# Kernel optimization log

Measured on AMD Instinct MI355X. Metric: run time of the kernel, lower is better.

Reference implementation:

```python
import jax, jax.numpy as jnp
import numpy as np

N, C, H, W = 1, 128, 512, 512
CH = C // 2  # channels seen by each 1x1 conv


def setup_inputs() -> dict:
    key = jax.random.key(0)
    ks = jax.random.split(key, 6)
    return {
        "lst": jax.random.normal(ks[0], (N, C, H, W), dtype=jnp.float32),
        "gui": jax.random.normal(ks[1], (N, C, H, W), dtype=jnp.float32),
        "w1": jax.random.normal(ks[2], (CH, CH), dtype=jnp.float32) * 0.05,  # conv1 weight (out,in) of 1x1 kernel
        "b1": jax.random.normal(ks[3], (CH,), dtype=jnp.float32) * 0.05,
        "w2": jax.random.normal(ks[4], (CH, CH), dtype=jnp.float32) * 0.05,  # conv2 weight
        "b2": jax.random.normal(ks[5], (CH,), dtype=jnp.float32) * 0.05,
        "p": 2,
    }


def _conv1x1(x, w, b):
    # x: [N, CH, H, W]; 1x1 conv == per-pixel channel mixing GEMM
    return jnp.einsum('oc,nchw->nohw', w, x) + b[None, :, None, None]


def reference(lst, gui, w1, b1, w2, b2, p):
    # channel_mask = arange(C) % p == 0 selects channels 0, p, 2p, ... -> strided slice [:, ::p]
    # Exchanged channels: out_lst gets conv2(gui_masked), out_gui gets conv1(lst_masked).
    # Unmasked channels pass through unchanged (out initialized as copy of input).
    out_lst = lst.at[:, ::p].set(_conv1x1(gui[:, ::p], w2, b2))
    out_gui = gui.at[:, ::p].set(_conv1x1(lst[:, ::p], w1, b1))
    return (out_lst, out_gui)
```

## Files before the change

### kernel.cpp

```cpp
#include <hip/hip_runtime.h>

#define HW (512 * 512)
#define CH 64
#define CONV_BLOCKS 1024
#define COPY_BLOCKS 4096
#define COPY_THREADS (COPY_BLOCKS * 256)
#define COPY_R 4

__global__ __launch_bounds__(256) void fused_exchange_kernel(
    const float* __restrict__ lst, const float* __restrict__ gui,
    const float* __restrict__ w1, const float* __restrict__ b1,
    const float* __restrict__ w2, const float* __restrict__ b2,
    float* __restrict__ out_lst, float* __restrict__ out_gui)
{
    const int b = blockIdx.x;

    if (b < CONV_BLOCKS) {
        const int pix = b * 256 + threadIdx.x;

        {
            float acc[CH];
            #pragma unroll
            for (int k = 0; k < CH; ++k) acc[k] = b2[k];

            for (int cc = 0; cc < CH; cc += 8) {
                float x[8];
                #pragma unroll
                for (int j = 0; j < 8; ++j)
                    x[j] = gui[(size_t)(2 * (cc + j)) * HW + pix];
                #pragma unroll
                for (int k = 0; k < CH; ++k) {
                    const float* wr = w2 + k * CH + cc;
                    float a = acc[k];
                    a = fmaf(wr[0], x[0], a);
                    a = fmaf(wr[1], x[1], a);
                    a = fmaf(wr[2], x[2], a);
                    a = fmaf(wr[3], x[3], a);
                    a = fmaf(wr[4], x[4], a);
                    a = fmaf(wr[5], x[5], a);
                    a = fmaf(wr[6], x[6], a);
                    a = fmaf(wr[7], x[7], a);
                    acc[k] = a;
                }
            }
            #pragma unroll
            for (int k = 0; k < CH; ++k)
                out_lst[(size_t)(2 * k) * HW + pix] = acc[k];
        }

        {
            float acc[CH];
            #pragma unroll
            for (int k = 0; k < CH; ++k) acc[k] = b1[k];

            for (int cc = 0; cc < CH; cc += 8) {
                float x[8];
                #pragma unroll
                for (int j = 0; j < 8; ++j)
                    x[j] = lst[(size_t)(2 * (cc + j)) * HW + pix];
                #pragma unroll
                for (int k = 0; k < CH; ++k) {
                    const float* wr = w1 + k * CH + cc;
                    float a = acc[k];
                    a = fmaf(wr[0], x[0], a);
                    a = fmaf(wr[1], x[1], a);
                    a = fmaf(wr[2], x[2], a);
                    a = fmaf(wr[3], x[3], a);
                    a = fmaf(wr[4], x[4], a);
                    a = fmaf(wr[5], x[5], a);
                    a = fmaf(wr[6], x[6], a);
                    a = fmaf(wr[7], x[7], a);
                    acc[k] = a;
                }
            }
            #pragma unroll
            for (int k = 0; k < CH; ++k)
                out_gui[(size_t)(2 * k) * HW + pix] = acc[k];
        }
    } else {
        const int t = (b - CONV_BLOCKS) * 256 + threadIdx.x;
        const float4* l4  = (const float4*)lst;
        const float4* g4  = (const float4*)gui;
        float4* ol4 = (float4*)out_lst;
        float4* og4 = (float4*)out_gui;

        #pragma unroll
        for (int r = 0; r < COPY_R; ++r) {
            const int idx = t + r * COPY_THREADS;
            const int c   = idx >> 16;
            const int j   = idx & 0xFFFF;
            const int off = ((2 * c + 1) << 16) + j;
            ol4[off] = l4[off];
            og4[off] = g4[off];
        }
    }
}

extern "C" void kernel_launch(void* const* d_in, const int* in_sizes, int n_in,
                              void* d_out, int out_size, void* d_ws, size_t ws_size,
                              hipStream_t stream) {
    const float* lst = (const float*)d_in[0];
    const float* gui = (const float*)d_in[1];
    const float* w1  = (const float*)d_in[2];
    const float* b1  = (const float*)d_in[3];
    const float* w2  = (const float*)d_in[4];
    const float* b2  = (const float*)d_in[5];

    float* out_lst = (float*)d_out;
    float* out_gui = out_lst + (size_t)128 * HW;

    fused_exchange_kernel<<<CONV_BLOCKS + COPY_BLOCKS, 256, 0, stream>>>(
        lst, gui, w1, b1, w2, b2, out_lst, out_gui);
}
```

Measured before the change: 553.2 us.

## Split conv output channels across waves with float2 pixels and uniform copy work

Restructures the fused kernel so each block handles 128 pixels, with each of four waves computing 16 output channels over two pixels per lane (float2). Weight addresses become wave-uniform via readfirstlane, so weights can live in scalar loads. Input channel loads are software-prefetched one chunk ahead. Every block now does both convs plus a slice of the passthrough copy instead of splitting conv and copy blocks, and launch bounds ask for higher occupancy. Each wave re-reads the same inputs, four times per block, which trades redundant loads for far lower register pressure.

```diff
diff --git a/kernel.cpp b/kernel.cpp
--- a/kernel.cpp
+++ b/kernel.cpp
@@ -2,96 +2,83 @@
 
 #define HW (512 * 512)
 #define CH 64
-#define CONV_BLOCKS 1024
-#define COPY_BLOCKS 4096
-#define COPY_THREADS (COPY_BLOCKS * 256)
-#define COPY_R 4
+#define NBLK 2048
+#define PIXB 128
+#define COPY_R 16
 
-__global__ __launch_bounds__(256) void fused_exchange_kernel(
+__global__ __launch_bounds__(256, 4) void fused_exchange_kernel(
     const float* __restrict__ lst, const float* __restrict__ gui,
     const float* __restrict__ w1, const float* __restrict__ b1,
     const float* __restrict__ w2, const float* __restrict__ b2,
     float* __restrict__ out_lst, float* __restrict__ out_gui)
 {
-    const int b = blockIdx.x;
+    const int b    = blockIdx.x;
+    const int tid  = threadIdx.x;
+    const int lane = tid & 63;
+    const int kg   = __builtin_amdgcn_readfirstlane(tid >> 6);
+    const int pix  = b * PIXB + lane * 2;
 
-    if (b < CONV_BLOCKS) {
-        const int pix = b * 256 + threadIdx.x;
+    auto conv_pass = [&](const float* __restrict__ src, const float* __restrict__ w,
+                         const float* __restrict__ bias, float* __restrict__ dst) {
+        const float* wbase = w + (size_t)(kg * 16) * CH;
 
-        {
-            float acc[CH];
-            #pragma unroll
-            for (int k = 0; k < CH; ++k) acc[k] = b2[k];
-
-            for (int cc = 0; cc < CH; cc += 8) {
-                float x[8];
-                #pragma unroll
-                for (int j = 0; j < 8; ++j)
-                    x[j] = gui[(size_t)(2 * (cc + j)) * HW + pix];
-                #pragma unroll
-                for (int k = 0; k < CH; ++k) {
-                    const float* wr = w2 + k * CH + cc;
-                    float a = acc[k];
-                    a = fmaf(wr[0], x[0], a);
-                    a = fmaf(wr[1], x[1], a);
-                    a = fmaf(wr[2], x[2], a);
-                    a = fmaf(wr[3], x[3], a);
-                    a = fmaf(wr[4], x[4], a);
-                    a = fmaf(wr[5], x[5], a);
-                    a = fmaf(wr[6], x[6], a);
-                    a = fmaf(wr[7], x[7], a);
-                    acc[k] = a;
-                }
-            }
-            #pragma unroll
-            for (int k = 0; k < CH; ++k)
-                out_lst[(size_t)(2 * k) * HW + pix] = acc[k];
+        float2 acc[16];
+        #pragma unroll
+        for (int k = 0; k < 16; ++k) {
+            const float bb = bias[kg * 16 + k];
+            acc[k].x = bb; acc[k].y = bb;
         }
 
-        {
-            float acc[CH];
+        float2 x[8];
+        #pragma unroll
+        for (int j = 0; j < 8; ++j)
+            x[j] = *(const float2*)(src + (size_t)(2 * j) * HW + pix);
+
+        auto fma_chunk = [&](int c0, const float2* xv) {
             #pragma unroll
-            for (int k = 0; k < CH; ++k) acc[k] = b1[k];
+            for (int k = 0; k < 16; ++k) {
+                const float* wr = wbase + k * CH + c0;
+                float ax = acc[k].x, ay = acc[k].y;
+                #pragma unroll
+                for (int j = 0; j < 8; ++j) {
+                    ax = fmaf(wr[j], xv[j].x, ax);
+                    ay = fmaf(wr[j], xv[j].y, ay);
+                }
+                acc[k].x = ax; acc[k].y = ay;
+            }
+        };
 
-            for (int cc = 0; cc < CH; cc += 8) {
-                float x[8];
-                #pragma unroll
-                for (int j = 0; j < 8; ++j)
-                    x[j] = lst[(size_t)(2 * (cc + j)) * HW + pix];
-                #pragma unroll
-                for (int k = 0; k < CH; ++k) {
-                    const float* wr = w1 + k * CH + cc;
-                    float a = acc[k];
-                    a = fmaf(wr[0], x[0], a);
-                    a = fmaf(wr[1], x[1], a);
-                    a = fmaf(wr[2], x[2], a);
-                    a = fmaf(wr[3], x[3], a);
-                    a = fmaf(wr[4], x[4], a);
-                    a = fmaf(wr[5], x[5], a);
-                    a = fmaf(wr[6], x[6], a);
-                    a = fmaf(wr[7], x[7], a);
-                    acc[k] = a;
-                }
-            }
+        for (int c0 = 0; c0 < CH - 8; c0 += 8) {
+            float2 xn[8];
             #pragma unroll
-            for (int k = 0; k < CH; ++k)
-                out_gui[(size_t)(2 * k) * HW + pix] = acc[k];
+            for (int j = 0; j < 8; ++j)
+                xn[j] = *(const float2*)(src + (size_t)(2 * (c0 + 8 + j)) * HW + pix);
+            fma_chunk(c0, x);
+            #pragma unroll
+            for (int j = 0; j < 8; ++j) x[j] = xn[j];
         }
-    } else {
-        const int t = (b - CONV_BLOCKS) * 256 + threadIdx.x;
-        const float4* l4  = (const float4*)lst;
-        const float4* g4  = (const float4*)gui;
-        float4* ol4 = (float4*)out_lst;
-        float4* og4 = (float4*)out_gui;
+        fma_chunk(CH - 8, x);
+
+        #pragma unroll
+        for (int k = 0; k < 16; ++k)
+            *(float2*)(dst + (size_t)(2 * (kg * 16 + k)) * HW + pix) = acc[k];
+    };
+
+    conv_pass(gui, w2, b2, out_lst);
+    conv_pass(lst, w1, b1, out_gui);
+
+    {
+        const float4* src = (b < 1024) ? (const float4*)lst : (const float4*)gui;
+        float4*       dst = (b < 1024) ? (float4*)out_lst  : (float4*)out_gui;
+        const int base = (b & 1023) * (256 * COPY_R) + tid;
 
         #pragma unroll
         for (int r = 0; r < COPY_R; ++r) {
-            const int idx = t + r * COPY_THREADS;
+            const int idx = base + r * 256;
             const int c   = idx >> 16;
             const int j   = idx & 0xFFFF;
             const int off = ((2 * c + 1) << 16) + j;
-            ol4[off] = l4[off];
-            og4[off] = g4[off];
+            dst[off] = src[off];
         }
     }
 }
@@ -109,6 +96,6 @@
     float* out_lst = (float*)d_out;
     float* out_gui = out_lst + (size_t)128 * HW;
 
-    fused_exchange_kernel<<<CONV_BLOCKS + COPY_BLOCKS, 256, 0, stream>>>(
+    fused_exchange_kernel<<<NBLK, 256, 0, stream>>>(
         lst, gui, w1, b1, w2, b2, out_lst, out_gui);
 }
```

Result: slower. 684.7 us (+23.8%).
